# Kernel tuning notes

Hardware: AMD Instinct MI355X
Metric: run time of the kernel (lower is better)

The kernel has to match this reference:

```python
import jax, jax.numpy as jnp
import numpy as np

MIN_DEPTH = 0.1   # BaseConfig.MIN_DEPTH (assumed)
MAX_DEPTH = 100.0 # BaseConfig.MAX_DEPTH (assumed)
SIGMA = 0.5
KERNEL_SIZE = 3


def setup_inputs() -> dict:
    key = jax.random.key(0)
    k1, k2, k3, k4 = jax.random.split(key, 4)
    B, N = 8, 4096  # B = batch*views
    pred_depth = jax.random.uniform(k1, (B, N), jnp.float32, 0.5, 10.0)
    ray_3d = jax.random.normal(k2, (B, N, 3), jnp.float32)
    # Conv1d(1, 1, kernel_size=3) parameters: weight (out=1, in=1, k), bias (1,)
    fan_in = 1 * KERNEL_SIZE
    bound = 1.0 / np.sqrt(fan_in)
    conv_w = jax.random.uniform(k3, (1, 1, KERNEL_SIZE), jnp.float32, -bound, bound)
    conv_b = jax.random.uniform(k4, (1,), jnp.float32, -bound, bound)
    global_scale = jnp.ones((1,), jnp.float32)
    return {"pred_depth": pred_depth, "ray_3d": ray_3d,
            "conv_w": conv_w, "conv_b": conv_b, "global_scale": global_scale}


def reference(pred_depth, ray_3d, conv_w, conv_b, global_scale):
    # pred_depth: (B, N); ray_3d: (B, N, 3)
    scaled = pred_depth * global_scale  # global scale (broadcast scalar param)

    # Conv1d(1->1, k=3, padding=1) over the point axis. NCW / OIW layouts.
    x = scaled[:, None, :]  # (B, 1, N)
    pad = KERNEL_SIZE // 2
    sm = jax.lax.conv_general_dilated(
        x, conv_w, window_strides=(1,), padding=[(pad, pad)],
        dimension_numbers=("NCW", "OIW", "NCW"))
    smoothed = sm[:, 0, :] + conv_b  # (B, N)

    # Pairwise squared Euclidean distances (== cdist(..)**2), computed directly.
    sq = jnp.sum(ray_3d * ray_3d, axis=-1)  # (B, N)
    inner = jnp.einsum("bnd,bmd->bnm", ray_3d, ray_3d)  # (B, N, N)
    d2 = jnp.maximum(sq[:, :, None] + sq[:, None, :] - 2.0 * inner, 0.0)

    # Gaussian kernel weights and weighted depth aggregation (bmm).
    w = jnp.exp(-d2 / (2.0 * SIGMA * SIGMA))  # (B, N, N)
    weighted = jnp.einsum("bnm,bm->bn", w, smoothed)  # (B, N)

    return jnp.clip(weighted, MIN_DEPTH, MAX_DEPTH)
```

## Files before the change

### kernel.cpp

```cpp
#include <hip/hip_runtime.h>
#include <math.h>

#define NFULL 4096
#define BATCH 8
#define LOG2E 1.44269504088896340736f

#define GSPLIT 64
#define MC (NFULL / GSPLIT)
#define NPT 4

typedef float v2f __attribute__((ext_vector_type(2)));

#if __has_builtin(__builtin_amdgcn_exp2f)
#define EXP2(x) __builtin_amdgcn_exp2f(x)
#else
#define EXP2(x) exp2f(x)
#endif

__global__ __launch_bounds__(256) void prep_kernel(
    const float* __restrict__ pred, const float* __restrict__ ray,
    const float* __restrict__ cw, const float* __restrict__ cb,
    const float* __restrict__ gs, float4* __restrict__ pm)
{
    int idx = blockIdx.x * 256 + threadIdx.x;
    int b = idx >> 12, n = idx & (NFULL - 1);
    float g  = gs[0];
    float w0 = cw[0], w1 = cw[1], w2 = cw[2], bias = cb[0];
    const float* pd = pred + b * NFULL;
    float pm1 = (n > 0)         ? pd[n - 1] : 0.f;
    float p0  = pd[n];
    float pp1 = (n < NFULL - 1) ? pd[n + 1] : 0.f;
    float sm = g * (w0 * pm1 + w1 * p0 + w2 * pp1) + bias;

    const float* r = ray + (size_t)idx * 3;
    float x = r[0], y = r[1], z = r[2];
    float sq = x * x + y * y + z * z;
    float sp = -2.f * LOG2E * sq;
    float shat = sm * EXP2(sp + 64.f);

    const float K = 2.4022448f;
    pm[idx] = make_float4(K * x, K * y, K * z, shat);
}

__global__ __launch_bounds__(256, 8) void pairs_kernel(
    const float4* __restrict__ pm, float* __restrict__ partial)
{
    int tid  = threadIdx.x;
    int lane = tid & 63;
    int wv   = tid >> 6;
    int e  = blockIdx.x;
    int g  = e & (GSPLIT - 1);
    int w2 = e >> 6;
    int nt = w2 & 3;
    int b  = w2 >> 2;

    const float4* P = pm + b * NFULL;
    int n0 = nt * 1024 + wv * 256 + lane;

    v2f ax[2], ay[2], az[2], Cn[2], acc[2];
#pragma unroll
    for (int p = 0; p < 2; ++p) {
        float4 a0 = P[n0 + 64 * (2 * p)];
        float4 a1 = P[n0 + 64 * (2 * p + 1)];
        ax[p] = (v2f){a0.x, a1.x};
        ay[p] = (v2f){a0.y, a1.y};
        az[p] = (v2f){a0.z, a1.z};
        v2f sq = __builtin_elementwise_fma(ax[p], ax[p],
                 __builtin_elementwise_fma(ay[p], ay[p], az[p] * az[p]));
        Cn[p] = -0.5f * sq - 64.f;
        acc[p] = (v2f){0.f, 0.f};
    }

    int m0 = g * MC;
#pragma unroll 8
    for (int m = m0; m < m0 + MC; ++m) {
        float4 q = P[m];
#pragma unroll
        for (int p = 0; p < 2; ++p) {
            v2f t = __builtin_elementwise_fma(ax[p], (v2f){q.x, q.x}, Cn[p]);
            t = __builtin_elementwise_fma(ay[p], (v2f){q.y, q.y}, t);
            t = __builtin_elementwise_fma(az[p], (v2f){q.z, q.z}, t);
            v2f ee = (v2f){EXP2(t.x), EXP2(t.y)};
            acc[p] = __builtin_elementwise_fma(ee, (v2f){q.w, q.w}, acc[p]);
        }
    }

    float* outp = partial + (size_t)g * (BATCH * NFULL) + b * NFULL;
#pragma unroll
    for (int p = 0; p < 2; ++p) {
        outp[n0 + 64 * (2 * p)]     = acc[p].x;
        outp[n0 + 64 * (2 * p + 1)] = acc[p].y;
    }
}

__global__ __launch_bounds__(256) void reduce_kernel(
    const float4* __restrict__ partial, float4* __restrict__ out)
{
    int idx = blockIdx.x * 256 + threadIdx.x;
    float4 s = make_float4(0.f, 0.f, 0.f, 0.f);
#pragma unroll
    for (int gg = 0; gg < GSPLIT; ++gg) {
        float4 v = partial[(size_t)gg * (BATCH * NFULL / 4) + idx];
        s.x += v.x; s.y += v.y; s.z += v.z; s.w += v.w;
    }
    float4 r;
    r.x = fminf(fmaxf(s.x, 0.1f), 100.f);
    r.y = fminf(fmaxf(s.y, 0.1f), 100.f);
    r.z = fminf(fmaxf(s.z, 0.1f), 100.f);
    r.w = fminf(fmaxf(s.w, 0.1f), 100.f);
    out[idx] = r;
}

extern "C" void kernel_launch(void* const* d_in, const int* in_sizes, int n_in,
                              void* d_out, int out_size, void* d_ws, size_t ws_size,
                              hipStream_t stream) {
    const float* pred = (const float*)d_in[0];
    const float* ray  = (const float*)d_in[1];
    const float* cw   = (const float*)d_in[2];
    const float* cb   = (const float*)d_in[3];
    const float* gs   = (const float*)d_in[4];

    float4* pm      = (float4*)d_ws;
    float*  partial = (float*)((char*)d_ws + (size_t)BATCH * NFULL * sizeof(float4));

    prep_kernel<<<BATCH * NFULL / 256, 256, 0, stream>>>(pred, ray, cw, cb, gs, pm);
    pairs_kernel<<<BATCH * 4 * GSPLIT, 256, 0, stream>>>(pm, partial);
    reduce_kernel<<<BATCH * NFULL / 1024, 256, 0, stream>>>(
        (const float4*)partial, (float4*)d_out);
}
```

Measured before the change: 87.29 us.

## Fuse prep kernel into pairs kernel with shared-memory column tile

```diff
diff --git a/kernel.cpp b/kernel.cpp
--- a/kernel.cpp
+++ b/kernel.cpp
@@ -7,7 +7,6 @@
 
 #define GSPLIT 64
 #define MC (NFULL / GSPLIT)
-#define NPT 4
 
 typedef float v2f __attribute__((ext_vector_type(2)));
 
@@ -17,34 +16,13 @@
 #define EXP2(x) exp2f(x)
 #endif
 
-__global__ __launch_bounds__(256) void prep_kernel(
+__global__ __launch_bounds__(256, 8) void pairs_kernel(
     const float* __restrict__ pred, const float* __restrict__ ray,
     const float* __restrict__ cw, const float* __restrict__ cb,
-    const float* __restrict__ gs, float4* __restrict__ pm)
+    const float* __restrict__ gs, float* __restrict__ partial)
 {
-    int idx = blockIdx.x * 256 + threadIdx.x;
-    int b = idx >> 12, n = idx & (NFULL - 1);
-    float g  = gs[0];
-    float w0 = cw[0], w1 = cw[1], w2 = cw[2], bias = cb[0];
-    const float* pd = pred + b * NFULL;
-    float pm1 = (n > 0)         ? pd[n - 1] : 0.f;
-    float p0  = pd[n];
-    float pp1 = (n < NFULL - 1) ? pd[n + 1] : 0.f;
-    float sm = g * (w0 * pm1 + w1 * p0 + w2 * pp1) + bias;
+    __shared__ float4 Q[MC];
 
-    const float* r = ray + (size_t)idx * 3;
-    float x = r[0], y = r[1], z = r[2];
-    float sq = x * x + y * y + z * z;
-    float sp = -2.f * LOG2E * sq;
-    float shat = sm * EXP2(sp + 64.f);
-
-    const float K = 2.4022448f;
-    pm[idx] = make_float4(K * x, K * y, K * z, shat);
-}
-
-__global__ __launch_bounds__(256, 8) void pairs_kernel(
-    const float4* __restrict__ pm, float* __restrict__ partial)
-{
     int tid  = threadIdx.x;
     int lane = tid & 63;
     int wv   = tid >> 6;
@@ -54,27 +32,41 @@
     int nt = w2 & 3;
     int b  = w2 >> 2;
 
-    const float4* P = pm + b * NFULL;
+    const float K = 2.4022448f;
+
+    if (tid < MC) {
+        int m = g * MC + tid;
+        const float* pd = pred + b * NFULL;
+        float pm1 = (m > 0)         ? pd[m - 1] : 0.f;
+        float p0  = pd[m];
+        float pp1 = (m < NFULL - 1) ? pd[m + 1] : 0.f;
+        float sm = gs[0] * (cw[0] * pm1 + cw[1] * p0 + cw[2] * pp1) + cb[0];
+
+        const float* r = ray + (size_t)(b * NFULL + m) * 3;
+        float x = r[0], y = r[1], z = r[2];
+        float sp = -2.f * LOG2E * (x * x + y * y + z * z);
+        Q[tid] = make_float4(K * x, K * y, K * z, sm * EXP2(sp + 64.f));
+    }
+
     int n0 = nt * 1024 + wv * 256 + lane;
-
     v2f ax[2], ay[2], az[2], Cn[2], acc[2];
 #pragma unroll
     for (int p = 0; p < 2; ++p) {
-        float4 a0 = P[n0 + 64 * (2 * p)];
-        float4 a1 = P[n0 + 64 * (2 * p + 1)];
-        ax[p] = (v2f){a0.x, a1.x};
-        ay[p] = (v2f){a0.y, a1.y};
-        az[p] = (v2f){a0.z, a1.z};
+        const float* r0 = ray + (size_t)(b * NFULL + n0 + 64 * (2 * p)) * 3;
+        const float* r1 = ray + (size_t)(b * NFULL + n0 + 64 * (2 * p + 1)) * 3;
+        ax[p] = (v2f){K * r0[0], K * r1[0]};
+        ay[p] = (v2f){K * r0[1], K * r1[1]};
+        az[p] = (v2f){K * r0[2], K * r1[2]};
         v2f sq = __builtin_elementwise_fma(ax[p], ax[p],
                  __builtin_elementwise_fma(ay[p], ay[p], az[p] * az[p]));
         Cn[p] = -0.5f * sq - 64.f;
         acc[p] = (v2f){0.f, 0.f};
     }
+    __syncthreads();
 
-    int m0 = g * MC;
 #pragma unroll 8
-    for (int m = m0; m < m0 + MC; ++m) {
-        float4 q = P[m];
+    for (int m = 0; m < MC; ++m) {
+        float4 q = Q[m];
 #pragma unroll
         for (int p = 0; p < 2; ++p) {
             v2f t = __builtin_elementwise_fma(ax[p], (v2f){q.x, q.x}, Cn[p]);
@@ -120,11 +112,9 @@
     const float* cb   = (const float*)d_in[3];
     const float* gs   = (const float*)d_in[4];
 
-    float4* pm      = (float4*)d_ws;
-    float*  partial = (float*)((char*)d_ws + (size_t)BATCH * NFULL * sizeof(float4));
+    float* partial = (float*)d_ws;
 
-    prep_kernel<<<BATCH * NFULL / 256, 256, 0, stream>>>(pred, ray, cw, cb, gs, pm);
-    pairs_kernel<<<BATCH * 4 * GSPLIT, 256, 0, stream>>>(pm, partial);
+    pairs_kernel<<<BATCH * 4 * GSPLIT, 256, 0, stream>>>(pred, ray, cw, cb, gs, partial);
     reduce_kernel<<<BATCH * NFULL / 1024, 256, 0, stream>>>(
         (const float4*)partial, (float4*)d_out);
 }
```

Result: no change. 86.67 us (-0.7%).
